# Kernel tuning notes

Measured on AMD Instinct MI355X. Metric: run time of the kernel, lower is better.

The kernel has to match this reference:

```python
import jax, jax.numpy as jnp
import numpy as np

C_REG = 0.1
MAX_ITER = 15
FEAT_SCALE = 0.05  # keep linear-kernel magnitudes moderate (encoder features are not unit randn)


def _boundary_alpha(v, dv):
    # largest step a s.t. v + a*dv >= 0, per batch element
    safe = jnp.where(dv < 0, dv, -1.0)
    r = jnp.where(dv < 0, -v / safe, jnp.inf)
    return jnp.min(r, axis=-1, keepdims=True)


def _svm_cs_qp(G, e, h, A, max_iter):
    """Batched primal-dual (Mehrotra) interior-point solve of
       min_z 0.5 z'Gz + e'z  s.t.  z <= h (C = I),  A z = 0,
    the Crammer-Singer dual QP solved by qpth.QPFunction in the original code."""
    B, n, _ = G.shape
    p = A.shape[0]
    eye_n = jnp.eye(n, dtype=G.dtype)
    Ab = jnp.broadcast_to(A, (B, p, n))
    At = jnp.swapaxes(Ab, 1, 2)
    zeros_pp = jnp.zeros((B, p, p), dtype=G.dtype)

    z0 = h - 1.0            # slack s = h - z = 1 > 0 (infeasible start for Az=0)
    s0 = jnp.ones_like(h)
    lam0 = jnp.ones_like(h)
    nu0 = jnp.zeros((B, p), dtype=G.dtype)

    def step(carry, _):
        z, s, lam, nu = carry
        Dls = lam / s
        r_d = jnp.einsum('bij,bj->bi', G, z) + e + lam + jnp.einsum('pn,bp->bn', A, nu)
        r_p = jnp.einsum('pn,bn->bp', A, z)
        mu = jnp.mean(s * lam, axis=-1, keepdims=True)
        # KKT matrix [[G + diag(lam/s), A'], [A, 0]]
        top = jnp.concatenate([G + Dls[:, :, None] * eye_n, At], axis=2)
        bot = jnp.concatenate([Ab, zeros_pp], axis=2)
        M = jnp.concatenate([top, bot], axis=1)  # (B, n+p, n+p)

        def ksolve(rhs1):
            rhs = jnp.concatenate([rhs1, -r_p], axis=1)
            sol = jnp.linalg.solve(M, rhs[..., None])[..., 0]
            return sol[:, :n], sol[:, n:]

        # predictor (affine) step, sigma = 0
        dz_a, _ = ksolve(-r_d + lam)
        ds_a = -dz_a
        dlam_a = -lam + Dls * dz_a
        a_aff = jnp.minimum(1.0, jnp.minimum(_boundary_alpha(s, ds_a), _boundary_alpha(lam, dlam_a)))
        mu_aff = jnp.mean((s + a_aff * ds_a) * (lam + a_aff * dlam_a), axis=-1, keepdims=True)
        sigma = (mu_aff / mu) ** 3
        # corrector step
        r_c = sigma * mu - ds_a * dlam_a
        dz, dnu = ksolve(-r_d + lam - r_c / s)
        ds = -dz
        dlam = r_c / s - lam + Dls * dz
        a = 0.995 * jnp.minimum(1.0, jnp.minimum(_boundary_alpha(s, ds), _boundary_alpha(lam, dlam)))
        return (z + a * dz, s + a * ds, lam + a * dlam, nu + a * dnu), None

    (z, _, _, _), _ = jax.lax.scan(step, (z0, s0, lam0, nu0), None, length=max_iter)
    return z


def _svm_cs_head(query, support, labels_onehot, n_way, scale):
    B, ns, d = support.shape
    n = ns * n_way
    # block_kernel_matrix = kron(K, I_way) + I_n  (Kronecker-expanded Gram)
    K = jnp.einsum('bnd,bmd->bnm', support, support)
    Iw = jnp.eye(n_way, dtype=K.dtype)
    G = (K[:, :, None, :, None] * Iw[None, None, :, None, :]).reshape(B, n, n)
    G = G + jnp.eye(n, dtype=K.dtype)
    oh = labels_onehot.reshape(B, n)      # (n_support, n_way) flattened, matches kron ordering
    e = -oh
    h = C_REG * oh
    # A = kron(I_ns, ones(1, n_way)): sum of dual vars over ways per support sample = 0
    A = jnp.repeat(jnp.eye(ns, dtype=K.dtype), n_way, axis=1)  # (ns, n)
    z = _svm_cs_qp(G, e, h, A, MAX_ITER)
    qp_sol = z.reshape(B, ns, n_way)
    compat = jnp.einsum('bsd,bqd->bsq', support, query)
    logits = jnp.einsum('bsw,bsq->bqw', qp_sol, compat)
    return scale * logits


def setup_inputs() -> dict:
    B, n_way, n_shot, n_query, d = 128, 5, 5, 75, 2560
    ns = n_way * n_shot
    k1, k2 = jax.random.split(jax.random.key(0))
    query = jax.random.normal(k1, (B, n_query, d), dtype=jnp.float32) * FEAT_SCALE
    support = jax.random.normal(k2, (B, ns, d), dtype=jnp.float32) * FEAT_SCALE
    # make_nk_label: class labels 0..n_way-1, n_shot each, per episode
    support_labels = jnp.tile(jnp.repeat(jnp.arange(n_way, dtype=jnp.int32), n_shot)[None, :], (B, 1))
    scale = jnp.ones((1,), dtype=jnp.float32)
    return {"query": query, "support": support, "scale": scale,
            "support_labels": support_labels, "n_way": n_way, "n_shot": n_shot}


def reference(query, support, scale, support_labels, n_way, n_shot):
    oh = jax.nn.one_hot(support_labels, n_way, dtype=query.dtype)
    return _svm_cs_head(query, support, oh, n_way, scale)
```

## Files before the change

### kernel.cpp

```cpp
#include <hip/hip_runtime.h>
#include <utility>

constexpr int BB   = 128;
constexpr int NSUP = 25;
constexpr int NWAY = 5;
constexpr int NTOT = 125;
constexpr int NQ   = 75;
constexpr int DIM  = 2560;
constexpr int MAXIT = 15;

#define FMA4(acc, zz, v)                     \
  acc.x = fmaf(zz, v.x, acc.x);              \
  acc.y = fmaf(zz, v.y, acc.y);              \
  acc.z = fmaf(zz, v.z, acc.z);              \
  acc.w = fmaf(zz, v.w, acc.w)

#define DOT4(a, u, vv) a += u.x*vv.x + u.y*vv.y + u.z*vv.z + u.w*vv.w

__device__ __forceinline__ float frcp(float x) {
#if __has_builtin(__builtin_amdgcn_rcpf)
  return __builtin_amdgcn_rcpf(x);
#else
  return 1.0f / x;
#endif
}

template <int IMM>
__device__ __forceinline__ float swzb(float v) {
  return __uint_as_float(
      (unsigned)__builtin_amdgcn_ds_swizzle((int)__float_as_uint(v), IMM));
}
template <int K>
__device__ __forceinline__ float bcast32(float v) {
  return swzb<(K << 5)>(v);
}

__device__ __forceinline__ float bfly_sum(float v) {
#pragma unroll
  for (int m = 32; m; m >>= 1) v += __shfl_xor(v, m);
  return v;
}
__device__ __forceinline__ float bfly_min(float v) {
#pragma unroll
  for (int m = 32; m; m >>= 1) v = fminf(v, __shfl_xor(v, m));
  return v;
}

template <int K>
__device__ __forceinline__ void gj_step(float (&R)[25], int j) {
  float pk   = bcast32<K>(R[K]);
  float pinv = frcp(pk);
  bool  piv  = (j == K);
  float ph   = piv ? pinv : R[K] * pinv;
#pragma unroll
  for (int i = 0; i < 25; ++i) {
    if (i == K) continue;
    float f    = bcast32<K>(R[i]);
    float base = piv ? 0.0f : R[i];
    R[i] = fmaf(-f, ph, base);
  }
  R[K] = ph;
}
template <int... Ks>
__device__ __forceinline__ void gj25_all(float (&R)[25], int j,
                                         std::integer_sequence<int, Ks...>) {
  (gj_step<Ks>(R, j), ...);
}
__device__ __forceinline__ void gj25(float (&R)[25], int j) {
  gj25_all(R, j, std::make_integer_sequence<int, 25>{});
}

template <int O, int... Ms>
__device__ __forceinline__ float mv_part(const float (&row)[25], float x,
                                         std::integer_sequence<int, Ms...>) {
  float acc = 0.0f;
  ((acc = fmaf(row[O + Ms], bcast32<O + Ms>(x), acc)), ...);
  return acc;
}
__device__ __forceinline__ float mv25(const float (&row)[25], float x) {
  return mv_part<0>(row, x, std::make_integer_sequence<int, 13>{}) +
         mv_part<13>(row, x, std::make_integer_sequence<int, 12>{});
}

__global__ __launch_bounds__(256) void k_gram(const float* __restrict__ sup,
                                              float* __restrict__ Kpart) {
  const int b    = blockIdx.x;
  const int half = blockIdx.y;
  const int tid  = threadIdx.x;
  const int wv   = tid >> 6;
  const int ln   = tid & 63;

  __shared__ float tile[28][260];
  __shared__ float accb[4][49][16];

  for (int c = tid; c < 3 * 260; c += 256) tile[25 + c / 260][c % 260] = 0.0f;

  const float* S = sup + (size_t)b * NSUP * DIM + half * 1280;

  float acc[4][4];
#pragma unroll
  for (int x = 0; x < 4; ++x)
#pragma unroll
    for (int y = 0; y < 4; ++y) acc[x][y] = 0.0f;

  const int ti = ln / 7, tj = ln % 7;
  const int i0 = 4 * ti, j0 = 4 * tj;

  for (int ch = 0; ch < 5; ++ch) {
    __syncthreads();
    for (int q = tid; q < 1600; q += 256) {
      int rr = q >> 6, c4 = q & 63;
      float4 v = *(const float4*)(S + rr * DIM + ch * 256 + 4 * c4);
      *(float4*)&tile[rr][4 * c4] = v;
    }
    __syncthreads();
    if (ln < 49) {
#pragma unroll
      for (int c = 0; c < 16; ++c) {
        const int d4 = (wv * 16 + c) * 4;
        float4 av[4], bv[4];
#pragma unroll
        for (int x = 0; x < 4; ++x) av[x] = *(const float4*)&tile[i0 + x][d4];
#pragma unroll
        for (int y = 0; y < 4; ++y) bv[y] = *(const float4*)&tile[j0 + y][d4];
#pragma unroll
        for (int x = 0; x < 4; ++x)
#pragma unroll
          for (int y = 0; y < 4; ++y) {
            acc[x][y] += av[x].x * bv[y].x + av[x].y * bv[y].y +
                         av[x].z * bv[y].z + av[x].w * bv[y].w;
          }
      }
    }
  }

  if (ln < 49) {
#pragma unroll
    for (int x = 0; x < 4; ++x)
#pragma unroll
      for (int y = 0; y < 4; ++y) accb[wv][ln][x * 4 + y] = acc[x][y];
  }
  __syncthreads();

  for (int p = tid; p < 625; p += 256) {
    int i = p / 25, jx = p % 25;
    int lx = (i / 4) * 7 + (jx / 4);
    int sx = (i % 4) * 4 + (jx % 4);
    float v = accb[0][lx][sx] + accb[1][lx][sx] + accb[2][lx][sx] + accb[3][lx][sx];
    Kpart[((size_t)half * BB + b) * 625 + p] = v;
  }
}

__global__ __launch_bounds__(192) void qp_solve3(const float* __restrict__ Kpart,
                                                 const int* __restrict__ labels,
                                                 float* __restrict__ zout) {
  const int b   = blockIdx.x;
  const int tid = threadIdx.x;
  const int wq  = tid >> 6;
  const int l   = tid & 63;
  const int h   = l >> 5;
  const int j   = l & 31;
  const bool act = (j < 25);
  const int jc  = act ? j : 0;
  const int matW = (wq == 2) ? 4 : 2 * wq + h;
  const bool cnt = act && !(wq == 2 && h == 1);

  __shared__ float Klds[25][26];
  __shared__ float Wlds[5][25][26];
  __shared__ float SL[25][26];
  __shared__ float Vb[5][28];
  __shared__ float Zl[5][28];
  __shared__ float NUl[28];
  __shared__ float MU[4], AA[4], PP[4], CC[4];

  for (int p = tid; p < 625; p += 192)
    Klds[p / 25][p % 25] =
        Kpart[(size_t)b * 625 + p] + Kpart[(size_t)(BB + b) * 625 + p];

  int lab = labels[b * 25 + jc];
  float oh = (lab == matW) ? 1.0f : 0.0f;
  float e_ = -oh;
  float z_ = 0.1f * oh - 1.0f;
  float s_ = 1.0f, lm_ = 1.0f;

  if (wq == 0 && h == 0 && act) NUl[jc] = 0.0f;
  if (cnt) Zl[matW][jc] = z_;
  {
    float sl = cnt ? s_ * lm_ : 0.0f;
    sl = bfly_sum(sl);
    if (l == 0) MU[wq] = sl;
  }
  __syncthreads();

  float Kc[25];
#pragma unroll
  for (int i = 0; i < 25; ++i) Kc[i] = Klds[i][jc];

  float R[25], Wrow[25], Srow[25];

#pragma unroll 1
  for (int it = 0; it < MAXIT; ++it) {
    float mu = (MU[0] + MU[1] + MU[2]) * (1.0f / 125.0f);
    float rp = Zl[0][jc] + Zl[1][jc] + Zl[2][jc] + Zl[3][jc] + Zl[4][jc];
    float nu = NUl[jc];
    float d_ = lm_ / s_;
    float kz = mv25(Kc, z_);
    float rd = kz + z_ + e_ + lm_ + nu;
    float rhs1 = lm_ - rd;

#pragma unroll
    for (int i = 0; i < 25; ++i) R[i] = Kc[i] + ((j == i) ? (1.0f + d_) : 0.0f);
    gj25(R, j);
    if (cnt) {
#pragma unroll
      for (int i = 0; i < 25; ++i) Wlds[matW][i][jc] = R[i];
    }
    __syncthreads();

#pragma unroll
    for (int m = 0; m < 25; ++m) Wrow[m] = Wlds[matW][jc][m];
    float v1 = mv25(Wrow, rhs1);
    if (cnt) Vb[matW][jc] = v1;

    if (wq == 0) {
#pragma unroll
      for (int i = 0; i < 25; ++i)
        R[i] = Wlds[0][i][jc] + Wlds[1][i][jc] + Wlds[2][i][jc] +
               Wlds[3][i][jc] + Wlds[4][i][jc];
      gj25(R, j);
      if (h == 0 && act) {
#pragma unroll
        for (int i = 0; i < 25; ++i) SL[i][jc] = R[i];
      }
    }
    __syncthreads();
#pragma unroll
    for (int m = 0; m < 25; ++m) Srow[m] = SL[jc][m];

    float u = Vb[0][jc] + Vb[1][jc] + Vb[2][jc] + Vb[3][jc] + Vb[4][jc];
    float t = u + rp;
    float dn1 = mv25(Srow, t);
    float r2 = rhs1 - dn1;
    float dz1 = mv25(Wrow, r2);
    float ds1 = -dz1;
    float dl1 = fmaf(d_, dz1, -lm_);
    float cand = 1.0f;
    if (act) {
      if (ds1 < 0.0f) cand = fminf(cand, -s_ / ds1);
      if (dl1 < 0.0f) cand = fminf(cand, -lm_ / dl1);
    }
    cand = bfly_min(cand);
    if (l == 0) AA[wq] = cand;
    __syncthreads();
    float a_aff = fminf(AA[0], fminf(AA[1], AA[2]));
    float pr = cnt ? (s_ + a_aff * ds1) * (lm_ + a_aff * dl1) : 0.0f;
    pr = bfly_sum(pr);
    if (l == 0) PP[wq] = pr;
    __syncthreads();
    float mu_aff = (PP[0] + PP[1] + PP[2]) * (1.0f / 125.0f);
    float rt = mu_aff / mu;
    float sg = rt * rt * rt * mu;

    float rc = sg - ds1 * dl1;
    float rhsc = lm_ - rd - rc / s_;
    float v2 = mv25(Wrow, rhsc);
    if (cnt) Vb[matW][jc] = v2;
    __syncthreads();
    float u2 = Vb[0][jc] + Vb[1][jc] + Vb[2][jc] + Vb[3][jc] + Vb[4][jc];
    float t2 = u2 + rp;
    float dn2 = mv25(Srow, t2);
    float r2c = rhsc - dn2;
    float dz2 = mv25(Wrow, r2c);
    float ds2 = -dz2;
    float dl2 = rc / s_ - lm_ + d_ * dz2;
    float c2 = 1.0f;
    if (act) {
      if (ds2 < 0.0f) c2 = fminf(c2, -s_ / ds2);
      if (dl2 < 0.0f) c2 = fminf(c2, -lm_ / dl2);
    }
    c2 = bfly_min(c2);
    if (l == 0) CC[wq] = c2;
    __syncthreads();
    float a = 0.995f * fminf(CC[0], fminf(CC[1], CC[2]));

    z_  = fmaf(a, dz2, z_);
    s_  = fmaf(a, ds2, s_);
    lm_ = fmaf(a, dl2, lm_);
    if (wq == 0 && h == 0 && act) NUl[jc] = nu + a * dn2;
    if (cnt) Zl[matW][jc] = z_;
    {
      float sl = cnt ? s_ * lm_ : 0.0f;
      sl = bfly_sum(sl);
      if (l == 0) MU[wq] = sl;
    }
    __syncthreads();
  }

  if (cnt) zout[(size_t)b * NTOT + jc * 5 + matW] = z_;
}

__global__ __launch_bounds__(256) void k_ws(const float* __restrict__ sup,
                                            const float* __restrict__ zsol,
                                            float* __restrict__ ws) {
  const int b   = blockIdx.x;
  const int tid = threadIdx.x;
  __shared__ float zsh[NTOT];
  if (tid < NTOT) zsh[tid] = zsol[(size_t)b * NTOT + tid];
  __syncthreads();

  const float* Sb = sup + (size_t)b * NSUP * DIM;
  for (int d4 = tid; d4 < 640; d4 += 256) {
    float4 a0 = {0,0,0,0}, a1 = {0,0,0,0}, a2 = {0,0,0,0}, a3 = {0,0,0,0}, a4 = {0,0,0,0};
#pragma unroll
    for (int s = 0; s < 25; ++s) {
      float4 v = *(const float4*)(Sb + s * DIM + 4 * d4);
      float z0 = zsh[s*5+0], z1 = zsh[s*5+1], z2 = zsh[s*5+2], z3 = zsh[s*5+3], z4 = zsh[s*5+4];
      FMA4(a0, z0, v); FMA4(a1, z1, v); FMA4(a2, z2, v); FMA4(a3, z3, v); FMA4(a4, z4, v);
    }
    float* W = ws + (size_t)b * NWAY * DIM;
    *(float4*)(W + 0*DIM + 4*d4) = a0;
    *(float4*)(W + 1*DIM + 4*d4) = a1;
    *(float4*)(W + 2*DIM + 4*d4) = a2;
    *(float4*)(W + 3*DIM + 4*d4) = a3;
    *(float4*)(W + 4*DIM + 4*d4) = a4;
  }
}

__global__ __launch_bounds__(256) void k_logits2(const float* __restrict__ query,
                                                 const float* __restrict__ scale,
                                                 const float* __restrict__ ws,
                                                 float* __restrict__ out) {
  const int b   = blockIdx.x;
  const int qt  = blockIdx.y;
  const int tid = threadIdx.x;
  const int wv  = tid >> 6, ln = tid & 63;

  __shared__ float wsb[5][2564];
  for (int p = tid; p < 3200; p += 256) {
    int w = p / 640, c = p % 640;
    *(float4*)&wsb[w][4 * c] = *(const float4*)(ws + ((size_t)b * NWAY + w) * DIM + 4 * c);
  }
  __syncthreads();

  const float sc = scale[0];
  const int q0 = qt * 15, q1 = q0 + 15;
  for (int q = q0 + wv; q < q1; q += 4) {
    const float* Q = query + ((size_t)b * NQ + q) * DIM;
    float a0 = 0.f, a1 = 0.f, a2 = 0.f, a3 = 0.f, a4 = 0.f;
#pragma unroll
    for (int c = 0; c < 10; ++c) {
      int d4 = (c * 64 + ln) * 4;
      float4 qv = *(const float4*)(Q + d4);
      float4 w0 = *(const float4*)&wsb[0][d4];
      float4 w1 = *(const float4*)&wsb[1][d4];
      float4 w2 = *(const float4*)&wsb[2][d4];
      float4 w3 = *(const float4*)&wsb[3][d4];
      float4 w4 = *(const float4*)&wsb[4][d4];
      DOT4(a0, qv, w0); DOT4(a1, qv, w1); DOT4(a2, qv, w2); DOT4(a3, qv, w3); DOT4(a4, qv, w4);
    }
#pragma unroll
    for (int off = 32; off; off >>= 1) {
      a0 += __shfl_xor(a0, off); a1 += __shfl_xor(a1, off); a2 += __shfl_xor(a2, off);
      a3 += __shfl_xor(a3, off); a4 += __shfl_xor(a4, off);
    }
    if (ln == 0) {
      float* O = out + ((size_t)b * NQ + q) * NWAY;
      O[0] = sc*a0; O[1] = sc*a1; O[2] = sc*a2; O[3] = sc*a3; O[4] = sc*a4;
    }
  }
}

__global__ __launch_bounds__(256) void k_logits(const float* __restrict__ sup,
                                                const float* __restrict__ query,
                                                const float* __restrict__ scale,
                                                const float* __restrict__ zsol,
                                                float* __restrict__ out) {
  const int b   = blockIdx.x;
  const int hq  = blockIdx.y;
  const int tid = threadIdx.x;

  __shared__ float wsb[5][2564];
  __shared__ float zsh[128];

  if (tid < NTOT) zsh[tid] = zsol[(size_t)b * NTOT + tid];
  __syncthreads();

  const float* Sb = sup + (size_t)b * NSUP * DIM;
  for (int d4 = tid; d4 < 640; d4 += 256) {
    float4 a0 = {0,0,0,0}, a1 = {0,0,0,0}, a2 = {0,0,0,0}, a3 = {0,0,0,0}, a4 = {0,0,0,0};
#pragma unroll
    for (int s = 0; s < 25; ++s) {
      float4 v = *(const float4*)(Sb + s * DIM + 4 * d4);
      float z0 = zsh[s*5+0], z1 = zsh[s*5+1], z2 = zsh[s*5+2], z3 = zsh[s*5+3], z4 = zsh[s*5+4];
      FMA4(a0, z0, v); FMA4(a1, z1, v); FMA4(a2, z2, v); FMA4(a3, z3, v); FMA4(a4, z4, v);
    }
    *(float4*)&wsb[0][4*d4] = a0; *(float4*)&wsb[1][4*d4] = a1; *(float4*)&wsb[2][4*d4] = a2;
    *(float4*)&wsb[3][4*d4] = a3; *(float4*)&wsb[4][4*d4] = a4;
  }
  __syncthreads();

  const float sc = scale[0];
  const int wv = tid >> 6, ln = tid & 63;
  const int q0 = hq * 38;
  const int q1 = (hq == 0) ? 38 : 75;

  for (int q = q0 + wv; q < q1; q += 4) {
    const float* Q = query + ((size_t)b * NQ + q) * DIM;
    float a0 = 0.f, a1 = 0.f, a2 = 0.f, a3 = 0.f, a4 = 0.f;
#pragma unroll
    for (int c = 0; c < 10; ++c) {
      int d4 = (c * 64 + ln) * 4;
      float4 qv = *(const float4*)(Q + d4);
      float4 w0 = *(const float4*)&wsb[0][d4];
      float4 w1 = *(const float4*)&wsb[1][d4];
      float4 w2 = *(const float4*)&wsb[2][d4];
      float4 w3 = *(const float4*)&wsb[3][d4];
      float4 w4 = *(const float4*)&wsb[4][d4];
      DOT4(a0, qv, w0); DOT4(a1, qv, w1); DOT4(a2, qv, w2); DOT4(a3, qv, w3); DOT4(a4, qv, w4);
    }
#pragma unroll
    for (int off = 32; off; off >>= 1) {
      a0 += __shfl_xor(a0, off); a1 += __shfl_xor(a1, off); a2 += __shfl_xor(a2, off);
      a3 += __shfl_xor(a3, off); a4 += __shfl_xor(a4, off);
    }
    if (ln == 0) {
      float* O = out + ((size_t)b * NQ + q) * NWAY;
      O[0] = sc*a0; O[1] = sc*a1; O[2] = sc*a2; O[3] = sc*a3; O[4] = sc*a4;
    }
  }
}

extern "C" void kernel_launch(void* const* d_in, const int* in_sizes, int n_in,
                              void* d_out, int out_size, void* d_ws, size_t ws_size,
                              hipStream_t stream) {
  (void)in_sizes; (void)n_in; (void)out_size;
  const float* query   = (const float*)d_in[0];
  const float* support = (const float*)d_in[1];
  const float* scale   = (const float*)d_in[2];
  const int*   labels  = (const int*)d_in[3];
  float* out = (float*)d_out;

  float* Kpart = (float*)d_ws;
  float* zsol  = Kpart + 2 * BB * 625;
  float* wsbuf = zsol + BB * NTOT;
  const size_t need = (size_t)(2*BB*625 + BB*NTOT + BB*NWAY*DIM) * 4;

  dim3 gA(BB, 2);
  k_gram<<<gA, 256, 0, stream>>>(support, Kpart);

  qp_solve3<<<dim3(BB), 192, 0, stream>>>(Kpart, labels, zsol);

  if (ws_size >= need) {
    k_ws<<<dim3(BB), 256, 0, stream>>>(support, zsol, wsbuf);
    k_logits2<<<dim3(BB, 5), 256, 0, stream>>>(query, scale, wsbuf, out);
  } else {
    k_logits<<<dim3(BB, 2), 256, 0, stream>>>(support, query, scale, zsol, out);
  }
}
```

Before: 557.1 us.

## Restructure QP solver to one wave per class with readlane broadcasts

Result: faster. 522.4 us (-6.2%).

```diff
diff --git a/kernel.cpp b/kernel.cpp
--- a/kernel.cpp
+++ b/kernel.cpp
@@ -1,5 +1,4 @@
 #include <hip/hip_runtime.h>
-#include <utility>
 
 constexpr int BB   = 128;
 constexpr int NSUP = 25;
@@ -25,14 +24,8 @@
 #endif
 }
 
-template <int IMM>
-__device__ __forceinline__ float swzb(float v) {
-  return __uint_as_float(
-      (unsigned)__builtin_amdgcn_ds_swizzle((int)__float_as_uint(v), IMM));
-}
-template <int K>
-__device__ __forceinline__ float bcast32(float v) {
-  return swzb<(K << 5)>(v);
+__device__ __forceinline__ float rlane(float v, int sl) {
+  return __uint_as_float(__builtin_amdgcn_readlane(__float_as_uint(v), (unsigned)sl));
 }
 
 __device__ __forceinline__ float bfly_sum(float v) {
@@ -47,39 +40,40 @@
 }
 
 template <int K>
-__device__ __forceinline__ void gj_step(float (&R)[25], int j) {
-  float pk   = bcast32<K>(R[K]);
-  float pinv = frcp(pk);
+__device__ __forceinline__ void gj_step_rl(float (&R)[25], int j) {
+  float pinv = frcp(rlane(R[K], K));
   bool  piv  = (j == K);
   float ph   = piv ? pinv : R[K] * pinv;
 #pragma unroll
   for (int i = 0; i < 25; ++i) {
     if (i == K) continue;
-    float f    = bcast32<K>(R[i]);
+    float f    = rlane(R[i], K);
     float base = piv ? 0.0f : R[i];
     R[i] = fmaf(-f, ph, base);
   }
   R[K] = ph;
 }
-template <int... Ks>
-__device__ __forceinline__ void gj25_all(float (&R)[25], int j,
-                                         std::integer_sequence<int, Ks...>) {
-  (gj_step<Ks>(R, j), ...);
+
+template <int K>
+__device__ __forceinline__ void gj25_rec(float (&R)[25], int j) {
+  gj_step_rl<K>(R, j);
+  if constexpr (K + 1 < 25) gj25_rec<K + 1>(R, j);
 }
 __device__ __forceinline__ void gj25(float (&R)[25], int j) {
-  gj25_all(R, j, std::make_integer_sequence<int, 25>{});
-}
-
-template <int O, int... Ms>
-__device__ __forceinline__ float mv_part(const float (&row)[25], float x,
-                                         std::integer_sequence<int, Ms...>) {
-  float acc = 0.0f;
-  ((acc = fmaf(row[O + Ms], bcast32<O + Ms>(x), acc)), ...);
-  return acc;
-}
-__device__ __forceinline__ float mv25(const float (&row)[25], float x) {
-  return mv_part<0>(row, x, std::make_integer_sequence<int, 13>{}) +
-         mv_part<13>(row, x, std::make_integer_sequence<int, 12>{});
+  gj25_rec<0>(R, j);
+}
+
+__device__ __forceinline__ float mv25rl(const float (&row)[25], float x) {
+  float a0 = 0.f, a1 = 0.f, a2 = 0.f, a3 = 0.f, a4 = 0.f;
+#pragma unroll
+  for (int m = 0; m < 5; ++m) {
+    a0 = fmaf(row[m],      rlane(x, m),      a0);
+    a1 = fmaf(row[5 + m],  rlane(x, 5 + m),  a1);
+    a2 = fmaf(row[10 + m], rlane(x, 10 + m), a2);
+    a3 = fmaf(row[15 + m], rlane(x, 15 + m), a3);
+    a4 = fmaf(row[20 + m], rlane(x, 20 + m), a4);
+  }
+  return ((a0 + a1) + (a2 + a3)) + a4;
 }
 
 __global__ __launch_bounds__(256) void k_gram(const float* __restrict__ sup,
@@ -151,97 +145,77 @@
   }
 }
 
-__global__ __launch_bounds__(192) void qp_solve3(const float* __restrict__ Kpart,
-                                                 const int* __restrict__ labels,
-                                                 float* __restrict__ zout) {
+__global__ __launch_bounds__(320, 1) void qp_solve5(const float* __restrict__ Kpart,
+                                                    const int* __restrict__ labels,
+                                                    float* __restrict__ zout) {
   const int b   = blockIdx.x;
   const int tid = threadIdx.x;
-  const int wq  = tid >> 6;
-  const int l   = tid & 63;
-  const int h   = l >> 5;
-  const int j   = l & 31;
+  const int w   = tid >> 6;
+  const int j   = tid & 63;
   const bool act = (j < 25);
   const int jc  = act ? j : 0;
-  const int matW = (wq == 2) ? 4 : 2 * wq + h;
-  const bool cnt = act && !(wq == 2 && h == 1);
 
   __shared__ float Klds[25][26];
-  __shared__ float Wlds[5][25][26];
-  __shared__ float SL[25][26];
+  __shared__ float WT[5][25][27];
+  __shared__ float Zl[5][28];
   __shared__ float Vb[5][28];
-  __shared__ float Zl[5][28];
-  __shared__ float NUl[28];
-  __shared__ float MU[4], AA[4], PP[4], CC[4];
-
-  for (int p = tid; p < 625; p += 192)
+  __shared__ float MU[8], AA[8], PP[8], CC[8];
+
+  for (int p = tid; p < 625; p += 320)
     Klds[p / 25][p % 25] =
         Kpart[(size_t)b * 625 + p] + Kpart[(size_t)(BB + b) * 625 + p];
 
   int lab = labels[b * 25 + jc];
-  float oh = (lab == matW) ? 1.0f : 0.0f;
+  float oh = (lab == w) ? 1.0f : 0.0f;
   float e_ = -oh;
   float z_ = 0.1f * oh - 1.0f;
-  float s_ = 1.0f, lm_ = 1.0f;
-
-  if (wq == 0 && h == 0 && act) NUl[jc] = 0.0f;
-  if (cnt) Zl[matW][jc] = z_;
+  float s_ = 1.0f, lm_ = 1.0f, nu_ = 0.0f;
+
+  if (act) Zl[w][jc] = z_;
   {
-    float sl = cnt ? s_ * lm_ : 0.0f;
+    float sl = act ? s_ * lm_ : 0.0f;
     sl = bfly_sum(sl);
-    if (l == 0) MU[wq] = sl;
+    if (j == 0) MU[w] = sl;
   }
   __syncthreads();
 
   float Kc[25];
 #pragma unroll
-  for (int i = 0; i < 25; ++i) Kc[i] = Klds[i][jc];
-
-  float R[25], Wrow[25], Srow[25];
+  for (int i = 0; i < 25; ++i) Kc[i] = Klds[jc][i];
+
+  float R[25], Sr[25];
 
 #pragma unroll 1
   for (int it = 0; it < MAXIT; ++it) {
-    float mu = (MU[0] + MU[1] + MU[2]) * (1.0f / 125.0f);
+    float mu = (MU[0] + MU[1] + MU[2] + MU[3] + MU[4]) * (1.0f / 125.0f);
     float rp = Zl[0][jc] + Zl[1][jc] + Zl[2][jc] + Zl[3][jc] + Zl[4][jc];
-    float nu = NUl[jc];
     float d_ = lm_ / s_;
-    float kz = mv25(Kc, z_);
-    float rd = kz + z_ + e_ + lm_ + nu;
+    float kz = mv25rl(Kc, z_);
+    float rd = kz + z_ + e_ + lm_ + nu_;
     float rhs1 = lm_ - rd;
 
 #pragma unroll
     for (int i = 0; i < 25; ++i) R[i] = Kc[i] + ((j == i) ? (1.0f + d_) : 0.0f);
     gj25(R, j);
-    if (cnt) {
-#pragma unroll
-      for (int i = 0; i < 25; ++i) Wlds[matW][i][jc] = R[i];
-    }
-    __syncthreads();
-
-#pragma unroll
-    for (int m = 0; m < 25; ++m) Wrow[m] = Wlds[matW][jc][m];
-    float v1 = mv25(Wrow, rhs1);
-    if (cnt) Vb[matW][jc] = v1;
-
-    if (wq == 0) {
-#pragma unroll
-      for (int i = 0; i < 25; ++i)
-        R[i] = Wlds[0][i][jc] + Wlds[1][i][jc] + Wlds[2][i][jc] +
-               Wlds[3][i][jc] + Wlds[4][i][jc];
-      gj25(R, j);
-      if (h == 0 && act) {
-#pragma unroll
-        for (int i = 0; i < 25; ++i) SL[i][jc] = R[i];
-      }
-    }
-    __syncthreads();
-#pragma unroll
-    for (int m = 0; m < 25; ++m) Srow[m] = SL[jc][m];
+    float v1 = mv25rl(R, rhs1);
+    if (act) {
+      Vb[w][jc] = v1;
+#pragma unroll
+      for (int i = 0; i < 25; ++i) WT[w][jc][i] = R[i];
+    }
+    __syncthreads();
+
+#pragma unroll
+    for (int i = 0; i < 25; ++i)
+      Sr[i] = WT[0][jc][i] + WT[1][jc][i] + WT[2][jc][i] +
+              WT[3][jc][i] + WT[4][jc][i];
+    gj25(Sr, j);
 
     float u = Vb[0][jc] + Vb[1][jc] + Vb[2][jc] + Vb[3][jc] + Vb[4][jc];
     float t = u + rp;
-    float dn1 = mv25(Srow, t);
+    float dn1 = mv25rl(Sr, t);
     float r2 = rhs1 - dn1;
-    float dz1 = mv25(Wrow, r2);
+    float dz1 = mv25rl(R, r2);
     float ds1 = -dz1;
     float dl1 = fmaf(d_, dz1, -lm_);
     float cand = 1.0f;
@@ -250,27 +224,27 @@
       if (dl1 < 0.0f) cand = fminf(cand, -lm_ / dl1);
     }
     cand = bfly_min(cand);
-    if (l == 0) AA[wq] = cand;
-    __syncthreads();
-    float a_aff = fminf(AA[0], fminf(AA[1], AA[2]));
-    float pr = cnt ? (s_ + a_aff * ds1) * (lm_ + a_aff * dl1) : 0.0f;
+    if (j == 0) AA[w] = cand;
+    __syncthreads();
+    float a_aff = fminf(fminf(fminf(AA[0], AA[1]), fminf(AA[2], AA[3])), AA[4]);
+    float pr = act ? (s_ + a_aff * ds1) * (lm_ + a_aff * dl1) : 0.0f;
     pr = bfly_sum(pr);
-    if (l == 0) PP[wq] = pr;
-    __syncthreads();
-    float mu_aff = (PP[0] + PP[1] + PP[2]) * (1.0f / 125.0f);
+    if (j == 0) PP[w] = pr;
+    __syncthreads();
+    float mu_aff = (PP[0] + PP[1] + PP[2] + PP[3] + PP[4]) * (1.0f / 125.0f);
     float rt = mu_aff / mu;
     float sg = rt * rt * rt * mu;
 
     float rc = sg - ds1 * dl1;
     float rhsc = lm_ - rd - rc / s_;
-    float v2 = mv25(Wrow, rhsc);
-    if (cnt) Vb[matW][jc] = v2;
+    float v2 = mv25rl(R, rhsc);
+    if (act) Vb[w][jc] = v2;
     __syncthreads();
     float u2 = Vb[0][jc] + Vb[1][jc] + Vb[2][jc] + Vb[3][jc] + Vb[4][jc];
     float t2 = u2 + rp;
-    float dn2 = mv25(Srow, t2);
+    float dn2 = mv25rl(Sr, t2);
     float r2c = rhsc - dn2;
-    float dz2 = mv25(Wrow, r2c);
+    float dz2 = mv25rl(R, r2c);
     float ds2 = -dz2;
     float dl2 = rc / s_ - lm_ + d_ * dz2;
     float c2 = 1.0f;
@@ -279,24 +253,24 @@
       if (dl2 < 0.0f) c2 = fminf(c2, -lm_ / dl2);
     }
     c2 = bfly_min(c2);
-    if (l == 0) CC[wq] = c2;
-    __syncthreads();
-    float a = 0.995f * fminf(CC[0], fminf(CC[1], CC[2]));
+    if (j == 0) CC[w] = c2;
+    __syncthreads();
+    float a = 0.995f * fminf(fminf(fminf(CC[0], CC[1]), fminf(CC[2], CC[3])), CC[4]);
 
     z_  = fmaf(a, dz2, z_);
     s_  = fmaf(a, ds2, s_);
     lm_ = fmaf(a, dl2, lm_);
-    if (wq == 0 && h == 0 && act) NUl[jc] = nu + a * dn2;
-    if (cnt) Zl[matW][jc] = z_;
+    nu_ = fmaf(a, dn2, nu_);
+    if (act) Zl[w][jc] = z_;
     {
-      float sl = cnt ? s_ * lm_ : 0.0f;
+      float sl = act ? s_ * lm_ : 0.0f;
       sl = bfly_sum(sl);
-      if (l == 0) MU[wq] = sl;
-    }
-    __syncthreads();
-  }
-
-  if (cnt) zout[(size_t)b * NTOT + jc * 5 + matW] = z_;
+      if (j == 0) MU[w] = sl;
+    }
+    __syncthreads();
+  }
+
+  if (act) zout[(size_t)b * NTOT + jc * 5 + w] = z_;
 }
 
 __global__ __launch_bounds__(256) void k_ws(const float* __restrict__ sup,
@@ -448,7 +422,7 @@
   dim3 gA(BB, 2);
   k_gram<<<gA, 256, 0, stream>>>(support, Kpart);
 
-  qp_solve3<<<dim3(BB), 192, 0, stream>>>(Kpart, labels, zsol);
+  qp_solve5<<<dim3(BB), 320, 0, stream>>>(Kpart, labels, zsol);
 
   if (ws_size >= need) {
     k_ws<<<dim3(BB), 256, 0, stream>>>(support, zsol, wsbuf);
```
